# Kernel optimization log

Measured on AMD Instinct MI355X. Metric: run time of the kernel, lower is better.

## Reference

```python
import jax, jax.numpy as jnp
import numpy as np

EMBED_DIM = 1024
NUM_HEADS = 16
HEAD_DIM = EMBED_DIM // NUM_HEADS
SEG_LENS = [1024, 2048, 4096]
DIL_RATIOS = [1, 2, 4]
NEG = -1e8  # lse fill value used by sparse_to_dense


def setup_inputs() -> dict:
    root = jax.random.key(0)
    ks = jax.random.split(root, 12)
    B, L, E = 1, 4096, EMBED_DIM
    s = 0.02
    return {
        "query": jax.random.normal(ks[0], (B, L, E), jnp.float32),
        "key": jax.random.normal(ks[1], (B, L, E), jnp.float32),
        "value": jax.random.normal(ks[2], (B, L, E), jnp.float32),
        "Wq": jax.random.normal(ks[3], (E, E), jnp.float32) * s,
        "bq": jnp.zeros((E,), jnp.float32),
        "Wk": jax.random.normal(ks[4], (E, E), jnp.float32) * s,
        "bk": jnp.zeros((E,), jnp.float32),
        "Wv": jax.random.normal(ks[5], (E, E), jnp.float32) * s,
        "bv": jnp.zeros((E,), jnp.float32),
        "Wo": jax.random.normal(ks[6], (E, E), jnp.float32) * s,
        "bo": jnp.zeros((E,), jnp.float32),
    }


def _branch(q, k, v, sl, dr, L):
    """One (segment_length, dilated_ratio) branch.
    q,k,v: (B, L, H, D). Returns dense out (B, H, L, D) and lse (B, H, L).
    """
    B = q.shape[0]
    H, D = NUM_HEADS, HEAD_DIM
    sl = min(sl, L)
    pad = (-L) % sl
    if pad:
        pw = ((0, 0), (0, pad), (0, 0), (0, 0))
        q, k, v = jnp.pad(q, pw), jnp.pad(k, pw), jnp.pad(v, pw)
    n = (L + pad) // sl  # segments
    qs = q.reshape(B * n, sl, H, D)
    ks = k.reshape(B * n, sl, H, D)
    vs = v.reshape(B * n, sl, H, D)
    # dense_to_sparse: head j (group r = j // (H//dr)) keeps positions i*dr + r
    hg = H // dr
    g = sl // dr
    grp = jnp.arange(H) // hg                      # (H,)
    pos = jnp.arange(g)[:, None] * dr + grp[None]  # (g, H) dense positions
    hidx = jnp.arange(H)[None, :]
    sp = lambda x: x[:, pos, hidx, :]              # (B*n, g, H, D)
    qd, kd, vd = sp(qs), sp(ks), sp(vs)
    # causal attention within each sparse segment (flash_attn semantics)
    scores = jnp.einsum('bqhd,bkhd->bhqk', qd, kd) * (D ** -0.5)
    mask = jnp.tril(jnp.ones((g, g), bool))
    scores = jnp.where(mask, scores, -jnp.inf)
    lse = jax.nn.logsumexp(scores, axis=-1)        # (B*n, H, g)
    o = jnp.einsum('bhqk,bkhd->bqhd', jnp.exp(scores - lse[..., None]), vd)
    # sparse_to_dense: scatter back onto dense positions, NEG elsewhere
    hcol = jnp.arange(H)[:, None]                  # (H,1)
    od = jnp.zeros((B * n, H, sl, D), o.dtype).at[:, hcol, pos.T].set(
        o.transpose(0, 2, 1, 3))
    ld = jnp.zeros((B * n, H, sl), lse.dtype).at[:, hcol, pos.T].set(lse)
    ld = jnp.where(ld == 0.0, NEG, ld)  # matches masked_fill_(lse == 0, -1e8)
    od = od.reshape(B, n, H, sl, D).transpose(0, 2, 1, 3, 4)
    od = od.reshape(B, H, n * sl, D)[:, :, :L]
    ld = ld.reshape(B, n, H, sl).transpose(0, 2, 1, 3).reshape(B, H, n * sl)[:, :, :L]
    return od, ld


def reference(query, key, value, Wq, bq, Wk, bk, Wv, bv, Wo, bo):
    B, L, E = query.shape
    H, D = NUM_HEADS, HEAD_DIM
    q = (query @ Wq.T + bq).reshape(B, L, H, D)
    k = (key @ Wk.T + bk).reshape(B, L, H, D)
    v = (value @ Wv.T + bv).reshape(B, L, H, D)
    outs, lses = [], []
    for sl, dr in zip(SEG_LENS, DIL_RATIOS):
        o, l = _branch(q, k, v, sl, dr, L)
        outs.append(o)
        lses.append(l)
    lse_all = jnp.stack(lses, 0)[..., None]        # (nb, B, H, L, 1)
    m = lse_all.max(0)
    w = jnp.exp(lse_all - m)
    w = w / w.sum(0)                               # softmax merge weights
    w = jax.lax.stop_gradient(w)                   # torch computes under no_grad
    out = sum(o * wi.astype(o.dtype) for o, wi in zip(outs, w))  # (B,H,L,D)
    out = out.transpose(0, 2, 1, 3).reshape(B, L, E)
    return out @ Wo.T + bo
```

## Files before the change

kernel.cpp:

```cpp
#include <hip/hip_runtime.h>
#include <math.h>


#define L_SEQ 4096
#define EDIM  1024
#define NH    16
#define HD    64
#define GLEN  1024

typedef __bf16 bf16;
typedef __bf16 bf16x8 __attribute__((ext_vector_type(8)));
typedef __bf16 bf16x4 __attribute__((ext_vector_type(4)));
typedef short  s16x4  __attribute__((ext_vector_type(4)));
typedef float  f32x4  __attribute__((ext_vector_type(4)));

__device__ __forceinline__ void gload16(const bf16* g, bf16* l) {
  __builtin_amdgcn_global_load_lds(
      (__attribute__((address_space(1))) void*)(const_cast<bf16*>(g)),
      (__attribute__((address_space(3))) void*)(l),
      16, 0, 0);
}

__device__ __forceinline__ f32x4 mfma16x16x16_bf16(bf16x4 a, bf16x4 b, f32x4 c) {
#if defined(__HIP_DEVICE_COMPILE__)
  union { bf16x4 h; s16x4 s; } ua, ub;
  ua.h = a; ub.h = b;
  return __builtin_amdgcn_mfma_f32_16x16x16bf16_1k(ua.s, ub.s, c, 0, 0, 0);
#else
  (void)a; (void)b;
  return c;
#endif
}

__global__ __launch_bounds__(256) void cvt_kernel(
    const float* q, const float* k, const float* v,
    const float* wq, const float* wk, const float* wv, const float* wo,
    bf16* oq, bf16* ok, bf16* ov,
    bf16* owq, bf16* owk, bf16* owv, bf16* owo)
{
  const float* src; bf16* dst; int n;
  switch (blockIdx.y) {
    case 0: src = q;  dst = oq;  n = L_SEQ*EDIM; break;
    case 1: src = k;  dst = ok;  n = L_SEQ*EDIM; break;
    case 2: src = v;  dst = ov;  n = L_SEQ*EDIM; break;
    case 3: src = wq; dst = owq; n = EDIM*EDIM; break;
    case 4: src = wk; dst = owk; n = EDIM*EDIM; break;
    case 5: src = wv; dst = owv; n = EDIM*EDIM; break;
    default: src = wo; dst = owo; n = EDIM*EDIM; break;
  }
  int i = (blockIdx.x * 256 + threadIdx.x) * 8;
  if (i >= n) return;
  const float4* s4 = (const float4*)(src + i);
  float4 a = s4[0], b = s4[1];
  bf16x8 o = { (bf16)a.x, (bf16)a.y, (bf16)a.z, (bf16)a.w,
               (bf16)b.x, (bf16)b.y, (bf16)b.z, (bf16)b.w };
  *(bf16x8*)(dst + i) = o;
}

template <typename OutT>
__device__ __forceinline__ void gemm_body(const bf16* __restrict__ A,
                                          const bf16* __restrict__ W,
                                          const float* __restrict__ bias,
                                          OutT* __restrict__ C)
{
  constexpr int K = 1024;
  __shared__ __align__(16) bf16 lA[128 * 32];
  __shared__ __align__(16) bf16 lB[128 * 32];

  const int tid  = threadIdx.x;
  const int lane = tid & 63;
  const int w    = tid >> 6;
  const int quad = lane >> 4;
  const int l16  = lane & 15;
  const int wr   = w >> 1, wc = w & 1;
  const int row0 = blockIdx.y * 128;
  const int col0 = blockIdx.x * 128;

  f32x4 acc[4][4] = {};

  const int c0 = tid, c1 = tid + 256;
  const bf16* Ab0 = A + (size_t)(row0 + (c0 >> 2)) * K + (c0 & 3) * 8;
  const bf16* Ab1 = A + (size_t)(row0 + (c1 >> 2)) * K + (c1 & 3) * 8;
  const bf16* Bb0 = W + (size_t)(col0 + (c0 >> 2)) * K + (c0 & 3) * 8;
  const bf16* Bb1 = W + (size_t)(col0 + (c1 >> 2)) * K + (c1 & 3) * 8;
  bf16* lA0 = &lA[c0 * 8]; bf16* lA1 = &lA[c1 * 8];
  bf16* lB0 = &lB[c0 * 8]; bf16* lB1 = &lB[c1 * 8];

  for (int kt = 0; kt < K; kt += 32) {
    __syncthreads();
    gload16(Ab0 + kt, lA0);
    gload16(Ab1 + kt, lA1);
    gload16(Bb0 + kt, lB0);
    gload16(Bb1 + kt, lB1);
    __syncthreads();

    bf16x8 af[4], bfrag[4];
#pragma unroll
    for (int mi = 0; mi < 4; mi++)
      af[mi] = *(const bf16x8*)&lA[(wr * 64 + mi * 16 + l16) * 32 + quad * 8];
#pragma unroll
    for (int ni = 0; ni < 4; ni++)
      bfrag[ni] = *(const bf16x8*)&lB[(wc * 64 + ni * 16 + l16) * 32 + quad * 8];
#pragma unroll
    for (int mi = 0; mi < 4; mi++)
#pragma unroll
      for (int ni = 0; ni < 4; ni++)
        acc[mi][ni] = __builtin_amdgcn_mfma_f32_16x16x32_bf16(
            af[mi], bfrag[ni], acc[mi][ni], 0, 0, 0);
  }

#pragma unroll
  for (int mi = 0; mi < 4; mi++) {
#pragma unroll
    for (int ni = 0; ni < 4; ni++) {
      const int gcol = col0 + wc * 64 + ni * 16 + l16;
      const float bv = bias[gcol];
#pragma unroll
      for (int r = 0; r < 4; r++) {
        const int grow = row0 + wr * 64 + mi * 16 + quad * 4 + r;
        C[(size_t)grow * 1024 + gcol] = (OutT)(acc[mi][ni][r] + bv);
      }
    }
  }
}

__global__ __launch_bounds__(256) void gemm_qkv_kernel(
    const bf16* xq, const bf16* xk, const bf16* xv,
    const bf16* wq, const bf16* wk, const bf16* wv,
    const float* bq, const float* bk, const float* bv,
    bf16* q, bf16* k, bf16* v)
{
  const bf16 *A, *W; const float* bias; bf16* C;
  if (blockIdx.z == 0)      { A = xq; W = wq; bias = bq; C = q; }
  else if (blockIdx.z == 1) { A = xk; W = wk; bias = bk; C = k; }
  else                      { A = xv; W = wv; bias = bv; C = v; }
  gemm_body<bf16>(A, W, bias, C);
}

__global__ __launch_bounds__(256) void gemm_out_kernel(
    const bf16* A, const bf16* W, const float* bias, float* C)
{
  gemm_body<float>(A, W, bias, C);
}

__global__ __launch_bounds__(256) void vtrans_kernel(
    const bf16* __restrict__ v, bf16* vt0, bf16* vt1, bf16* vt2)
{
  __shared__ __align__(16) bf16 ltile[64 * 72];
  const int bid = blockIdx.x;
  int sl, dr, rem, shift; bf16* vt;
  if (bid < 1024)      { sl = 1024; dr = 1; rem = bid;        vt = vt0; shift = 4; }
  else if (bid < 1536) { sl = 2048; dr = 2; rem = bid - 1024; vt = vt1; shift = 3; }
  else                 { sl = 4096; dr = 4; rem = bid - 1536; vt = vt2; shift = 2; }
  const int ktile = rem & 15;
  const int h     = (rem >> 4) & 15;
  const int seg   = rem >> 8;
  const int grp   = h >> shift;
  const int segbase = seg * sl;
  const int tid = threadIdx.x;
  {
    const int i = tid >> 2, dc = tid & 3;
    const size_t p = (size_t)(segbase + (ktile * 64 + i) * dr + grp);
    const bf16* src = v + p * EDIM + h * 64 + dc * 16;
    *(uint4*)&ltile[i * 72 + dc * 16]     = *(const uint4*)(src);
    *(uint4*)&ltile[i * 72 + dc * 16 + 8] = *(const uint4*)(src + 8);
  }
  __syncthreads();
  {
    const int d = tid >> 2, kc = tid & 3;
    __align__(16) bf16 tmp[16];
#pragma unroll
    for (int j = 0; j < 16; j++) tmp[j] = ltile[(kc * 16 + j) * 72 + d];
    bf16* dst = vt + ((size_t)(seg * NH + h) * 64 + d) * GLEN + ktile * 64 + kc * 16;
    *(uint4*)dst       = *(uint4*)&tmp[0];
    *(uint4*)(dst + 8) = *(uint4*)&tmp[8];
  }
}

__global__ __launch_bounds__(256) void attn_kernel(
    const bf16* __restrict__ qg, const bf16* __restrict__ kg,
    const bf16* vt0, const bf16* vt1, const bf16* vt2,
    bf16* o0, bf16* o1, bf16* o2,
    float* l0, float* l1, float* l2)
{
  __shared__ __align__(16) bf16 lK[2][64 * 64];
  __shared__ __align__(16) bf16 lV[2][64 * 64];

  const int bid = blockIdx.x;
  int sl, dr, rem, shift;
  const bf16* vt; bf16* ob; float* lseb;
  if (bid < 1024)      { sl = 1024; dr = 1; rem = bid;        vt = vt0; ob = o0; lseb = l0; shift = 4; }
  else if (bid < 1536) { sl = 2048; dr = 2; rem = bid - 1024; vt = vt1; ob = o1; lseb = l1; shift = 3; }
  else                 { sl = 4096; dr = 4; rem = bid - 1536; vt = vt2; ob = o2; lseb = l2; shift = 2; }
  const int qt  = 15 - (rem & 15);
  const int h   = (rem >> 4) & 15;
  const int seg = rem >> 8;
  const int grp = h >> shift;
  const int segbase = seg * sl;

  const int tid = threadIdx.x, lane = tid & 63, w = tid >> 6;
  const int quad = lane >> 4, l16 = lane & 15;
  const int qs0 = qt * 64;

  bf16x8 qa0, qa1;
  {
    const int qi = qs0 + w * 16 + l16;
    const size_t p = (size_t)(segbase + qi * dr + grp);
    const bf16* qp = qg + p * EDIM + h * 64 + quad * 8;
    qa0 = *(const bf16x8*)(qp);
    qa1 = *(const bf16x8*)(qp + 32);
  }

  f32x4 Oa[4] = {};
  float m_r = -__builtin_inff(), l_r = 0.f;

  const bf16* vbase = vt + (size_t)(seg * NH + h) * 64 * GLEN;
  const int c0 = tid, c1 = tid + 256;
  const int r0 = c0 >> 3, sw0 = ((c0 & 7) ^ (r0 & 7));
  const int r1 = c1 >> 3, sw1 = ((c1 & 7) ^ (r1 & 7));

  auto stage = [&](int kt, int buf) {
    const bf16* kp0 = kg + (size_t)(segbase + (kt * 64 + r0) * dr + grp) * EDIM + h * 64 + sw0 * 8;
    const bf16* kp1 = kg + (size_t)(segbase + (kt * 64 + r1) * dr + grp) * EDIM + h * 64 + sw1 * 8;
    gload16(kp0, &lK[buf][c0 * 8]);
    gload16(kp1, &lK[buf][c1 * 8]);
    const bf16* vp0 = vbase + (size_t)r0 * GLEN + kt * 64 + sw0 * 8;
    const bf16* vp1 = vbase + (size_t)r1 * GLEN + kt * 64 + sw1 * 8;
    gload16(vp0, &lV[buf][c0 * 8]);
    gload16(vp1, &lV[buf][c1 * 8]);
  };

  stage(0, 0);

  const int qi_lane = qs0 + w * 16 + l16;

  for (int kt = 0; kt <= qt; kt++) {
    __syncthreads();
    if (kt < qt) stage(kt + 1, (kt + 1) & 1);
    const bf16* bK = lK[kt & 1];
    const bf16* bV = lV[kt & 1];

    const bool diag = (kt == qt);
    const int tmax = diag ? w : 3;

    f32x4 s[4];
#pragma unroll
    for (int t = 0; t < 4; t++) {
      if (t <= tmax) {
        s[t] = f32x4{0.f, 0.f, 0.f, 0.f};
        const int kj = t * 16 + l16;
        const int rs = kj & 7;
        bf16x8 ka0 = *(const bf16x8*)&bK[kj * 64 + ((quad       ^ rs) * 8)];
        bf16x8 ka1 = *(const bf16x8*)&bK[kj * 64 + (((4 + quad) ^ rs) * 8)];
        s[t] = __builtin_amdgcn_mfma_f32_16x16x32_bf16(ka0, qa0, s[t], 0, 0, 0);
        s[t] = __builtin_amdgcn_mfma_f32_16x16x32_bf16(ka1, qa1, s[t], 0, 0, 0);
      }
    }

    float p[4][4];
    float mloc = -__builtin_inff();
#pragma unroll
    for (int t = 0; t < 4; t++) {
      if (t <= tmax) {
#pragma unroll
        for (int r = 0; r < 4; r++) {
          float sv = s[t][r] * 0.125f;
          if (diag) {
            const int kj = kt * 64 + t * 16 + quad * 4 + r;
            if (kj > qi_lane) sv = -__builtin_inff();
          }
          p[t][r] = sv;
          mloc = fmaxf(mloc, sv);
        }
      }
    }
    mloc = fmaxf(mloc, __shfl_xor(mloc, 16, 64));
    mloc = fmaxf(mloc, __shfl_xor(mloc, 32, 64));
    const float mnew  = fmaxf(m_r, mloc);
    const float alpha = __expf(m_r - mnew);
    m_r = mnew;

    bf16x4 pb[4];
    float rs_sum = 0.f;
#pragma unroll
    for (int t = 0; t < 4; t++) {
      if (t <= tmax) {
#pragma unroll
        for (int r = 0; r < 4; r++) {
          const float pv = __expf(p[t][r] - mnew);
          pb[t][r] = (bf16)pv;
          rs_sum += pv;
        }
      }
    }
    rs_sum += __shfl_xor(rs_sum, 16, 64);
    rs_sum += __shfl_xor(rs_sum, 32, 64);
    l_r = l_r * alpha + rs_sum;

#pragma unroll
    for (int nf = 0; nf < 4; nf++) {
#pragma unroll
      for (int r = 0; r < 4; r++) Oa[nf][r] *= alpha;
    }

#pragma unroll
    for (int t = 0; t < 4; t++) {
      if (t <= tmax) {
        const int ck  = 2 * t + (quad >> 1);
        const int sub = (quad & 1) * 4;
#pragma unroll
        for (int nf = 0; nf < 4; nf++) {
          const int drow = nf * 16 + l16;
          bf16x4 va = *(const bf16x4*)&bV[drow * 64 + ((ck ^ (drow & 7)) * 8) + sub];
          Oa[nf] = mfma16x16x16_bf16(va, pb[t], Oa[nf]);
        }
      }
    }
  }

  const float linv = 1.0f / l_r;
  const int pdense = segbase + qi_lane * dr + grp;
  bf16* orow = ob + (size_t)pdense * EDIM + h * 64;
#pragma unroll
  for (int nf = 0; nf < 4; nf++) {
    bf16x4 ov;
#pragma unroll
    for (int r = 0; r < 4; r++) ov[r] = (bf16)(Oa[nf][r] * linv);
    *(bf16x4*)(orow + nf * 16 + quad * 4) = ov;
  }
  if (quad == 0)
    lseb[h * L_SEQ + pdense] = m_r + __logf(l_r);
}

__global__ __launch_bounds__(256) void merge_kernel(
    const bf16* __restrict__ o0, const bf16* __restrict__ o1, const bf16* __restrict__ o2,
    const float* __restrict__ l0, const float* __restrict__ l1, const float* __restrict__ l2,
    bf16* __restrict__ merged)
{
  const int idx = blockIdx.x * 256 + threadIdx.x;
  const int dc = idx & 7;
  const int h  = (idx >> 3) & 15;
  const int p  = idx >> 7;
  const bool c1 = ((p & 1) == (h >> 3));
  const bool c2 = ((p & 3) == (h >> 2));
  const float s0 = l0[h * L_SEQ + p];
  const float s1 = c1 ? l1[h * L_SEQ + p] : -__builtin_inff();
  const float s2 = c2 ? l2[h * L_SEQ + p] : -__builtin_inff();
  const float mx = fmaxf(s0, fmaxf(s1, s2));
  float w0 = __expf(s0 - mx);
  float w1 = c1 ? __expf(s1 - mx) : 0.f;
  float w2 = c2 ? __expf(s2 - mx) : 0.f;
  const float inv = 1.0f / (w0 + w1 + w2);
  w0 *= inv; w1 *= inv; w2 *= inv;

  const size_t off = (size_t)p * EDIM + h * 64 + dc * 8;
  float acc[8];
  bf16x8 a0 = *(const bf16x8*)(o0 + off);
#pragma unroll
  for (int j = 0; j < 8; j++) acc[j] = w0 * (float)a0[j];
  if (c1) {
    bf16x8 a1 = *(const bf16x8*)(o1 + off);
#pragma unroll
    for (int j = 0; j < 8; j++) acc[j] += w1 * (float)a1[j];
  }
  if (c2) {
    bf16x8 a2 = *(const bf16x8*)(o2 + off);
#pragma unroll
    for (int j = 0; j < 8; j++) acc[j] += w2 * (float)a2[j];
  }
  bf16x8 r;
#pragma unroll
  for (int j = 0; j < 8; j++) r[j] = (bf16)acc[j];
  *(bf16x8*)(merged + off) = r;
}

extern "C" void kernel_launch(void* const* d_in, const int* in_sizes, int n_in,
                              void* d_out, int out_size, void* d_ws, size_t ws_size,
                              hipStream_t stream)
{
  (void)in_sizes; (void)n_in; (void)out_size; (void)ws_size;
  const float* query = (const float*)d_in[0];
  const float* key   = (const float*)d_in[1];
  const float* value = (const float*)d_in[2];
  const float* Wq = (const float*)d_in[3];
  const float* bq = (const float*)d_in[4];
  const float* Wk = (const float*)d_in[5];
  const float* bk = (const float*)d_in[6];
  const float* Wv = (const float*)d_in[7];
  const float* bv = (const float*)d_in[8];
  const float* Wo = (const float*)d_in[9];
  const float* bo = (const float*)d_in[10];

  char* base = (char*)d_ws;
  size_t off = 0;
  auto take = [&](size_t nbytes) -> char* {
    char* p = base + off;
    off += (nbytes + 255) & ~(size_t)255;
    return p;
  };
  const size_t LE2 = (size_t)L_SEQ * EDIM * 2;
  const size_t EE2 = (size_t)EDIM * EDIM * 2;
  bf16* xq  = (bf16*)take(LE2);
  bf16* xk  = (bf16*)take(LE2);
  bf16* xv  = (bf16*)take(LE2);
  bf16* wqb = (bf16*)take(EE2);
  bf16* wkb = (bf16*)take(EE2);
  bf16* wvb = (bf16*)take(EE2);
  bf16* wob = (bf16*)take(EE2);
  bf16* qb  = (bf16*)take(LE2);
  bf16* kb  = (bf16*)take(LE2);
  bf16* vb  = (bf16*)take(LE2);
  bf16* vt0 = (bf16*)take((size_t)4 * NH * HD * GLEN * 2);
  bf16* vt1 = (bf16*)take((size_t)2 * NH * HD * GLEN * 2);
  bf16* vt2 = (bf16*)take((size_t)1 * NH * HD * GLEN * 2);
  float* lse0 = (float*)take((size_t)NH * L_SEQ * 4);
  float* lse1 = (float*)take((size_t)NH * L_SEQ * 4);
  float* lse2 = (float*)take((size_t)NH * L_SEQ * 4);
  bf16* merged = (bf16*)take(LE2);
  bf16* o0 = xq; bf16* o1 = xk; bf16* o2 = xv;

  dim3 blk(256);
  cvt_kernel<<<dim3(2048, 7), blk, 0, stream>>>(
      query, key, value, Wq, Wk, Wv, Wo, xq, xk, xv, wqb, wkb, wvb, wob);
  gemm_qkv_kernel<<<dim3(8, 32, 3), blk, 0, stream>>>(
      xq, xk, xv, wqb, wkb, wvb, bq, bk, bv, qb, kb, vb);
  vtrans_kernel<<<dim3(1792), blk, 0, stream>>>(vb, vt0, vt1, vt2);
  attn_kernel<<<dim3(1792), blk, 0, stream>>>(
      qb, kb, vt0, vt1, vt2, o0, o1, o2, lse0, lse1, lse2);
  merge_kernel<<<dim3(2048), blk, 0, stream>>>(
      o0, o1, o2, lse0, lse1, lse2, merged);
  gemm_out_kernel<<<dim3(8, 32), blk, 0, stream>>>(merged, wob, bo, (float*)d_out);
}
```

Baseline: 258.6 us.

## Pair causal query tiles per block, use exp2 softmax with lazy rescaling

Each attention block now processes two query tiles (qt and 15-qt), so the causal workload is balanced across blocks and each staged K/V tile is reused by both. The grid is halved and the block order is swizzled across XCDs. The softmax now works in the exp2 domain with the scale folded into one FMA, and the running output is rescaled only when the max grows by more than a threshold. This trims exp and multiply work, at the cost of more registers per thread (launch_bounds set to 4 blocks per CU) and possible fp32 overflow risk from the lazy-rescale bound.

```diff
diff --git a/kernel.cpp b/kernel.cpp
--- a/kernel.cpp
+++ b/kernel.cpp
@@ -29,6 +29,14 @@
 #else
   (void)a; (void)b;
   return c;
+#endif
+}
+
+__device__ __forceinline__ float fast_exp2(float x) {
+#if __has_builtin(__builtin_amdgcn_exp2f)
+  return __builtin_amdgcn_exp2f(x);
+#else
+  return __expf(x * 0.6931471805599453f);
 #endif
 }
 
@@ -177,7 +185,7 @@
   }
 }
 
-__global__ __launch_bounds__(256) void attn_kernel(
+__global__ __launch_bounds__(256, 4) void attn_kernel(
     const bf16* __restrict__ qg, const bf16* __restrict__ kg,
     const bf16* vt0, const bf16* vt1, const bf16* vt2,
     bf16* o0, bf16* o1, bf16* o2,
@@ -186,33 +194,39 @@
   __shared__ __align__(16) bf16 lK[2][64 * 64];
   __shared__ __align__(16) bf16 lV[2][64 * 64];
 
-  const int bid = blockIdx.x;
+  const int bid0 = blockIdx.x;
+  const int o = (bid0 & 7) * 112 + (bid0 >> 3);
+
   int sl, dr, rem, shift;
   const bf16* vt; bf16* ob; float* lseb;
-  if (bid < 1024)      { sl = 1024; dr = 1; rem = bid;        vt = vt0; ob = o0; lseb = l0; shift = 4; }
-  else if (bid < 1536) { sl = 2048; dr = 2; rem = bid - 1024; vt = vt1; ob = o1; lseb = l1; shift = 3; }
-  else                 { sl = 4096; dr = 4; rem = bid - 1536; vt = vt2; ob = o2; lseb = l2; shift = 2; }
-  const int qt  = 15 - (rem & 15);
-  const int h   = (rem >> 4) & 15;
-  const int seg = rem >> 8;
+  if (o < 512)      { sl = 1024; dr = 1; rem = o;       vt = vt0; ob = o0; lseb = l0; shift = 4; }
+  else if (o < 768) { sl = 2048; dr = 2; rem = o - 512; vt = vt1; ob = o1; lseb = l1; shift = 3; }
+  else              { sl = 4096; dr = 4; rem = o - 768; vt = vt2; ob = o2; lseb = l2; shift = 2; }
+  const int j   = rem & 7;
+  const int h   = (rem >> 3) & 15;
+  const int seg = rem >> 7;
+  const int qtA = 15 - j;
+  const int qtB = j;
   const int grp = h >> shift;
   const int segbase = seg * sl;
 
   const int tid = threadIdx.x, lane = tid & 63, w = tid >> 6;
   const int quad = lane >> 4, l16 = lane & 15;
-  const int qs0 = qt * 64;
-
-  bf16x8 qa0, qa1;
-  {
-    const int qi = qs0 + w * 16 + l16;
+
+  auto loadq = [&](int qt, bf16x8& a0, bf16x8& a1) {
+    const int qi = qt * 64 + w * 16 + l16;
     const size_t p = (size_t)(segbase + qi * dr + grp);
     const bf16* qp = qg + p * EDIM + h * 64 + quad * 8;
-    qa0 = *(const bf16x8*)(qp);
-    qa1 = *(const bf16x8*)(qp + 32);
-  }
-
-  f32x4 Oa[4] = {};
-  float m_r = -__builtin_inff(), l_r = 0.f;
+    a0 = *(const bf16x8*)(qp);
+    a1 = *(const bf16x8*)(qp + 32);
+  };
+  bf16x8 qaA0, qaA1, qaB0, qaB1;
+  loadq(qtA, qaA0, qaA1);
+  loadq(qtB, qaB0, qaB1);
+
+  f32x4 OA[4] = {}, OB[4] = {};
+  float mA = -__builtin_inff(), lAcc = 0.f;
+  float mB = -__builtin_inff(), lBcc = 0.f;
 
   const bf16* vbase = vt + (size_t)(seg * NH + h) * 64 * GLEN;
   const int c0 = tid, c1 = tid + 256;
@@ -230,17 +244,12 @@
     gload16(vp1, &lV[buf][c1 * 8]);
   };
 
-  stage(0, 0);
-
-  const int qi_lane = qs0 + w * 16 + l16;
-
-  for (int kt = 0; kt <= qt; kt++) {
-    __syncthreads();
-    if (kt < qt) stage(kt + 1, (kt + 1) & 1);
-    const bf16* bK = lK[kt & 1];
-    const bf16* bV = lV[kt & 1];
-
-    const bool diag = (kt == qt);
+  const float CS = 0.18033688011112042f;
+
+  auto tile_compute = [&](const bf16* bK, const bf16* bV,
+                          const bf16x8& qa0, const bf16x8& qa1,
+                          f32x4 (&Oa)[4], float& m_r, float& l_r,
+                          const bool diag, const int kt, const int qi_lane) {
     const int tmax = diag ? w : 3;
 
     f32x4 s[4];
@@ -257,28 +266,35 @@
       }
     }
 
-    float p[4][4];
-    float mloc = -__builtin_inff();
+    float mraw = -__builtin_inff();
 #pragma unroll
     for (int t = 0; t < 4; t++) {
       if (t <= tmax) {
 #pragma unroll
         for (int r = 0; r < 4; r++) {
-          float sv = s[t][r] * 0.125f;
+          float sv = s[t][r];
           if (diag) {
             const int kj = kt * 64 + t * 16 + quad * 4 + r;
             if (kj > qi_lane) sv = -__builtin_inff();
           }
-          p[t][r] = sv;
-          mloc = fmaxf(mloc, sv);
+          s[t][r] = sv;
+          mraw = fmaxf(mraw, sv);
         }
       }
     }
-    mloc = fmaxf(mloc, __shfl_xor(mloc, 16, 64));
-    mloc = fmaxf(mloc, __shfl_xor(mloc, 32, 64));
-    const float mnew  = fmaxf(m_r, mloc);
-    const float alpha = __expf(m_r - mnew);
-    m_r = mnew;
+    mraw = fmaxf(mraw, __shfl_xor(mraw, 16, 64));
+    mraw = fmaxf(mraw, __shfl_xor(mraw, 32, 64));
+    const float mloc = mraw * CS;
+    const float mnew = fmaxf(m_r, mloc);
+    if (mnew - m_r > 8.0f) {
+      const float alpha = fast_exp2(m_r - mnew);
+#pragma unroll
+      for (int nf = 0; nf < 4; nf++)
+#pragma unroll
+        for (int r = 0; r < 4; r++) Oa[nf][r] *= alpha;
+      l_r *= alpha;
+      m_r = mnew;
+    }
 
     bf16x4 pb[4];
     float rs_sum = 0.f;
@@ -287,7 +303,7 @@
       if (t <= tmax) {
 #pragma unroll
         for (int r = 0; r < 4; r++) {
-          const float pv = __expf(p[t][r] - mnew);
+          const float pv = fast_exp2(__builtin_fmaf(s[t][r], CS, -m_r));
           pb[t][r] = (bf16)pv;
           rs_sum += pv;
         }
@@ -295,13 +311,7 @@
     }
     rs_sum += __shfl_xor(rs_sum, 16, 64);
     rs_sum += __shfl_xor(rs_sum, 32, 64);
-    l_r = l_r * alpha + rs_sum;
-
-#pragma unroll
-    for (int nf = 0; nf < 4; nf++) {
-#pragma unroll
-      for (int r = 0; r < 4; r++) Oa[nf][r] *= alpha;
-    }
+    l_r += rs_sum;
 
 #pragma unroll
     for (int t = 0; t < 4; t++) {
@@ -316,20 +326,39 @@
         }
       }
     }
-  }
-
-  const float linv = 1.0f / l_r;
-  const int pdense = segbase + qi_lane * dr + grp;
-  bf16* orow = ob + (size_t)pdense * EDIM + h * 64;
-#pragma unroll
-  for (int nf = 0; nf < 4; nf++) {
-    bf16x4 ov;
-#pragma unroll
-    for (int r = 0; r < 4; r++) ov[r] = (bf16)(Oa[nf][r] * linv);
-    *(bf16x4*)(orow + nf * 16 + quad * 4) = ov;
-  }
-  if (quad == 0)
-    lseb[h * L_SEQ + pdense] = m_r + __logf(l_r);
+  };
+
+  const int qiA = qtA * 64 + w * 16 + l16;
+  const int qiB = qtB * 64 + w * 16 + l16;
+
+  stage(0, 0);
+  for (int kt = 0; kt <= qtA; kt++) {
+    __syncthreads();
+    if (kt < qtA) stage(kt + 1, (kt + 1) & 1);
+    const bf16* bK = lK[kt & 1];
+    const bf16* bV = lV[kt & 1];
+    tile_compute(bK, bV, qaA0, qaA1, OA, mA, lAcc, kt == qtA, kt, qiA);
+    if (kt <= qtB)
+      tile_compute(bK, bV, qaB0, qaB1, OB, mB, lBcc, kt == qtB, kt, qiB);
+  }
+
+  auto epilogue = [&](const f32x4 (&Oa)[4], float m_r, float l_r, int qt) {
+    const int qi = qt * 64 + w * 16 + l16;
+    const float linv = 1.0f / l_r;
+    const int pdense = segbase + qi * dr + grp;
+    bf16* orow = ob + (size_t)pdense * EDIM + h * 64;
+#pragma unroll
+    for (int nf = 0; nf < 4; nf++) {
+      bf16x4 ov;
+#pragma unroll
+      for (int r = 0; r < 4; r++) ov[r] = (bf16)(Oa[nf][r] * linv);
+      *(bf16x4*)(orow + nf * 16 + quad * 4) = ov;
+    }
+    if (quad == 0)
+      lseb[h * L_SEQ + pdense] = m_r * 0.6931471805599453f + __logf(l_r);
+  };
+  epilogue(OA, mA, lAcc, qtA);
+  epilogue(OB, mB, lBcc, qtB);
 }
 
 __global__ __launch_bounds__(256) void merge_kernel(
@@ -425,7 +454,7 @@
   gemm_qkv_kernel<<<dim3(8, 32, 3), blk, 0, stream>>>(
       xq, xk, xv, wqb, wkb, wvb, bq, bk, bv, qb, kb, vb);
   vtrans_kernel<<<dim3(1792), blk, 0, stream>>>(vb, vt0, vt1, vt2);
-  attn_kernel<<<dim3(1792), blk, 0, stream>>>(
+  attn_kernel<<<dim3(896), blk, 0, stream>>>(
       qb, kb, vt0, vt1, vt2, o0, o1, o2, lse0, lse1, lse2);
   merge_kernel<<<dim3(2048), blk, 0, stream>>>(
       o0, o1, o2, lse0, lse1, lse2, merged);
```

Measured after the change: 249.6 us. 1.04x faster.
